# Optimization experiments

Measured on AMD Instinct MI355X. Metric: run time of the kernel, lower is better.

The kernel has to match this reference:

```python
import jax, jax.numpy as jnp
import numpy as np

N_NODES = 50000
N_EDGES = 800000
D = 64


def setup_inputs() -> dict:
    key = jax.random.key(0)
    ks = jax.random.split(key, 8)
    scale = 1.0 / np.sqrt(D)
    x = jax.random.normal(ks[0], (N_NODES, D), dtype=jnp.float32)
    edge_index = jax.random.randint(ks[1], (2, N_EDGES), 0, N_NODES, dtype=jnp.int64)
    W1_root = jax.random.normal(ks[2], (D, D), dtype=jnp.float32) * scale
    W1_nbr = jax.random.normal(ks[3], (D, D), dtype=jnp.float32) * scale
    b1 = jnp.zeros((D,), dtype=jnp.float32)
    W2_root = jax.random.normal(ks[4], (D, D), dtype=jnp.float32) * scale
    W2_nbr = jax.random.normal(ks[5], (D, D), dtype=jnp.float32) * scale
    b2 = jnp.zeros((D,), dtype=jnp.float32)
    return {"x": x, "edge_index": edge_index,
            "W1_root": W1_root, "W1_nbr": W1_nbr, "b1": b1,
            "W2_root": W2_root, "W2_nbr": W2_nbr, "b2": b2}


def graph_conv(x, src, dst, W_root, W_nbr, b, n_nodes):
    # sum-aggregate neighbor features: msg j->i uses x[src], scattered to dst
    agg = jax.ops.segment_sum(x[src], dst, num_segments=n_nodes)  # [N, D]
    return x @ W_root + agg @ W_nbr + b


def reference(x, edge_index, W1_root, W1_nbr, b1, W2_root, W2_nbr, b2):
    src, dst = edge_index[0], edge_index[1]
    n = x.shape[0]
    h = jax.nn.relu(graph_conv(x, src, dst, W1_root, W1_nbr, b1, n))
    out = graph_conv(h, src, dst, W2_root, W2_nbr, b2, n)
    return out
```

## Files before the change

kernel.cpp:

```cpp
#include <hip/hip_runtime.h>

#define N_NODES 50000
#define N_EDGES 800000
#define D 64
#define NBUCKETS 782
#define NPB 64
#define BCAP 2048
#define SBLOCKS 256
#define CHUNK (N_EDGES / SBLOCKS)
#define MB ((N_NODES + 63) / 64)

__device__ __forceinline__ unsigned short f2bf(float f) {
    unsigned u = __float_as_uint(f);
    return (unsigned short)((u + 0x7fffu + ((u >> 16) & 1u)) >> 16);
}
__device__ __forceinline__ float bflo(unsigned u) {
    return __uint_as_float(u << 16);
}
__device__ __forceinline__ float bfhi(unsigned u) {
    return __uint_as_float(u & 0xffff0000u);
}

__device__ __forceinline__ void scatter_body(
    const int* __restrict__ src, const int* __restrict__ dst,
    int* __restrict__ cursorPad, int* __restrict__ staged,
    char* smem, int bid, int t) {
    int* hist = (int*)smem;
    int* curs = (int*)(smem + 3200);
    int* pk   = (int*)(smem + 6400);
    unsigned short* bk = (unsigned short*)(smem + 6400 + 12500);
    for (int i = t; i < NBUCKETS; i += 256) hist[i] = 0;
    __syncthreads();
    int lo = bid * CHUNK;
    for (int i = t; i < CHUNK; i += 256) {
        int d = dst[lo + i];
        int s = src[lo + i];
        pk[i] = (s << 6) | (d & 63);
        bk[i] = (unsigned short)(d >> 6);
        atomicAdd(&hist[d >> 6], 1);
    }
    __syncthreads();
    for (int k = t; k < NBUCKETS; k += 256)
        if (hist[k] > 0)
            curs[k] = k * BCAP + atomicAdd(&cursorPad[k * 16], hist[k]);
    __syncthreads();
    for (int i = t; i < CHUNK; i += 256) {
        int b = bk[i];
        int pos = atomicAdd(&curs[b], 1);
        staged[pos] = pk[i];
    }
}

__global__ void __launch_bounds__(256) csr_build_kernel(
    const int* __restrict__ cursorPad, const int* __restrict__ staged,
    int* __restrict__ csr, int* __restrict__ startA, int* __restrict__ endA) {
    __shared__ int deg[NPB];
    __shared__ int sc[NPB];
    __shared__ int curs[NPB];
    __shared__ int lcsr[BCAP];
    int k = blockIdx.x;
    int t = threadIdx.x;
    int base = k * BCAP;
    int cnt  = cursorPad[k * 16];
    if (t < NPB) deg[t] = 0;
    __syncthreads();
    for (int i = t; i < cnt; i += 256)
        atomicAdd(&deg[staged[base + i] & 63], 1);
    __syncthreads();
    int v = (t < NPB) ? deg[t] : 0;
    if (t < NPB) sc[t] = v;
    __syncthreads();
#pragma unroll
    for (int d = 1; d < NPB; d <<= 1) {
        int u = (t < NPB && t >= d) ? sc[t - d] : 0;
        __syncthreads();
        if (t < NPB) sc[t] += u;
        __syncthreads();
    }
    if (t < NPB) {
        int start = sc[t] - v;
        int node = k * NPB + t;
        if (node < N_NODES) {
            startA[node] = base + start;
            endA[node]   = base + start + v;
        }
        curs[t] = start;
    }
    __syncthreads();
    for (int i = t; i < cnt; i += 256) {
        int e = staged[base + i];
        int pos = atomicAdd(&curs[e & 63], 1);
        lcsr[pos] = e >> 6;
    }
    __syncthreads();
    for (int i = t; i < cnt; i += 256)
        csr[base + i] = lcsr[i];
}

template<int XBF>
__device__ __forceinline__ void gemm_body(
    const float* __restrict__ Xf, const unsigned short* __restrict__ Xb,
    const float* __restrict__ Wr, const float* __restrict__ Wn,
    float* __restrict__ outR, unsigned short* __restrict__ outN,
    int node0, int tid, char* smem) {
    float (*sXT)[D] = (float(*)[D])smem;
    float (*sWr)[D] = (float(*)[D])(smem + 16384);
    float (*sWn)[D] = (float(*)[D])(smem + 32768);

#pragma unroll
    for (int i = 0; i < 4; i++) {
        int idx = tid + 256 * i;
        ((float4*)sWr)[idx] = ((const float4*)Wr)[idx];
        ((float4*)sWn)[idx] = ((const float4*)Wn)[idx];
    }
    int nd = tid & 63;
    int gn = min(node0 + nd, N_NODES - 1);
    if (XBF) {
#pragma unroll
        for (int pass = 0; pass < 2; pass++) {
            int kg = (tid >> 6) + pass * 4;
            int k0 = kg * 8;
            uint4 ux = *(const uint4*)(Xb + (size_t)gn * D + k0);
            sXT[k0 + 0][nd] = bflo(ux.x); sXT[k0 + 1][nd] = bfhi(ux.x);
            sXT[k0 + 2][nd] = bflo(ux.y); sXT[k0 + 3][nd] = bfhi(ux.y);
            sXT[k0 + 4][nd] = bflo(ux.z); sXT[k0 + 5][nd] = bfhi(ux.z);
            sXT[k0 + 6][nd] = bflo(ux.w); sXT[k0 + 7][nd] = bfhi(ux.w);
        }
    } else {
        const float4* X4 = (const float4*)Xf;
#pragma unroll
        for (int pass = 0; pass < 4; pass++) {
            int kq = (tid >> 6) + pass * 4;
            float4 v = X4[gn * 16 + kq];
            sXT[kq * 4 + 0][nd] = v.x; sXT[kq * 4 + 1][nd] = v.y;
            sXT[kq * 4 + 2][nd] = v.z; sXT[kq * 4 + 3][nd] = v.w;
        }
    }
    __syncthreads();

    int nq = tid >> 4;
    int cq = tid & 15;
    float accR[4][4];
    float accN[4][4];
#pragma unroll
    for (int i = 0; i < 4; i++)
#pragma unroll
        for (int jj = 0; jj < 4; jj++) { accR[i][jj] = 0.f; accN[i][jj] = 0.f; }

#pragma unroll 16
    for (int k = 0; k < D; k++) {
        float4 xv = *(const float4*)&sXT[k][nq * 4];
        float4 wr = *(const float4*)&sWr[k][cq * 4];
        float4 wn = *(const float4*)&sWn[k][cq * 4];
        float xs[4] = {xv.x, xv.y, xv.z, xv.w};
        float rs[4] = {wr.x, wr.y, wr.z, wr.w};
        float ns[4] = {wn.x, wn.y, wn.z, wn.w};
#pragma unroll
        for (int i = 0; i < 4; i++)
#pragma unroll
            for (int jj = 0; jj < 4; jj++) {
                accR[i][jj] = fmaf(xs[i], rs[jj], accR[i][jj]);
                accN[i][jj] = fmaf(xs[i], ns[jj], accN[i][jj]);
            }
    }

    float4* outR4 = (float4*)outR;
#pragma unroll
    for (int i = 0; i < 4; i++) {
        int node = node0 + nq * 4 + i;
        if (node < N_NODES) {
            float4 r;
            r.x = accR[i][0]; r.y = accR[i][1];
            r.z = accR[i][2]; r.w = accR[i][3];
            outR4[node * 16 + cq] = r;
            ushort4 rb;
            rb.x = f2bf(accN[i][0]); rb.y = f2bf(accN[i][1]);
            rb.z = f2bf(accN[i][2]); rb.w = f2bf(accN[i][3]);
            *(ushort4*)(outN + (size_t)node * D + cq * 4) = rb;
        }
    }
}

__global__ void __launch_bounds__(256) scatter_gemm1(
    const int* __restrict__ src, const int* __restrict__ dst,
    int* __restrict__ cursorPad, int* __restrict__ staged,
    const float* __restrict__ X,
    const float* __restrict__ Wr, const float* __restrict__ Wn,
    float* __restrict__ xr, unsigned short* __restrict__ xn) {
    __shared__ char smem[49152];
    if (blockIdx.x < SBLOCKS) {
        scatter_body(src, dst, cursorPad, staged, smem, blockIdx.x, threadIdx.x);
    } else {
        gemm_body<0>(X, (const unsigned short*)0, Wr, Wn, xr, xn,
                     (blockIdx.x - SBLOCKS) * 64, threadIdx.x, smem);
    }
}

__global__ void __launch_bounds__(256) gemm2(
    const unsigned short* __restrict__ Xb,
    const float* __restrict__ Wr, const float* __restrict__ Wn,
    float* __restrict__ hr, unsigned short* __restrict__ hn) {
    __shared__ char smem[49152];
    gemm_body<1>((const float*)0, Xb, Wr, Wn, hr, hn,
                 blockIdx.x * 64, threadIdx.x, smem);
}

template<int RELU, int OUTBF>
__global__ void __launch_bounds__(256) gather_fused(
    const unsigned short* __restrict__ Gsrc, const float* __restrict__ Root,
    const float* __restrict__ bias,
    const int* __restrict__ startA, const int* __restrict__ endA,
    const int* __restrict__ csr,
    float* __restrict__ outF, unsigned short* __restrict__ outB) {
    int tid = threadIdx.x;
    int wave = tid >> 6, lane = tid & 63;
    int node = blockIdx.x * 4 + wave;
    int sub = lane >> 3, fq = lane & 7;
    int j0 = startA[node], je = endA[node];
    float a0=0.f,a1=0.f,a2=0.f,a3=0.f,a4=0.f,a5=0.f,a6=0.f,a7=0.f;
    for (int jb = j0; jb < je; jb += 64) {
        int idx = jb + lane;
        int p = csr[idx < je ? idx : (je - 1)];
        int m = min(64, je - jb);
        int b = 0;
        for (; b + 16 <= m; b += 16) {
            int i0 = __shfl(p, b + sub, 64);
            int i1 = __shfl(p, b + 8 + sub, 64);
            uint4 u0 = *(const uint4*)(Gsrc + i0 * D + fq * 8);
            uint4 u1 = *(const uint4*)(Gsrc + i1 * D + fq * 8);
            a0 += bflo(u0.x) + bflo(u1.x);  a1 += bfhi(u0.x) + bfhi(u1.x);
            a2 += bflo(u0.y) + bflo(u1.y);  a3 += bfhi(u0.y) + bfhi(u1.y);
            a4 += bflo(u0.z) + bflo(u1.z);  a5 += bfhi(u0.z) + bfhi(u1.z);
            a6 += bflo(u0.w) + bflo(u1.w);  a7 += bfhi(u0.w) + bfhi(u1.w);
        }
        for (; b < m; b += 8) {
            int sidx = b + sub;
            int scl = sidx < m ? sidx : (m - 1);
            int i0 = __shfl(p, scl, 64);
            if (sidx < m) {
                uint4 u = *(const uint4*)(Gsrc + i0 * D + fq * 8);
                a0 += bflo(u.x); a1 += bfhi(u.x);
                a2 += bflo(u.y); a3 += bfhi(u.y);
                a4 += bflo(u.z); a5 += bfhi(u.z);
                a6 += bflo(u.w); a7 += bfhi(u.w);
            }
        }
    }
#pragma unroll
    for (int mk = 8; mk <= 32; mk <<= 1) {
        a0 += __shfl_xor(a0, mk, 64); a1 += __shfl_xor(a1, mk, 64);
        a2 += __shfl_xor(a2, mk, 64); a3 += __shfl_xor(a3, mk, 64);
        a4 += __shfl_xor(a4, mk, 64); a5 += __shfl_xor(a5, mk, 64);
        a6 += __shfl_xor(a6, mk, 64); a7 += __shfl_xor(a7, mk, 64);
    }
    if (sub == 0) {
        const float* rp = Root + (size_t)node * D + fq * 8;
        float4 x0 = *(const float4*)rp;
        float4 x1 = *(const float4*)(rp + 4);
        float4 b0 = ((const float4*)bias)[fq * 2];
        float4 b1 = ((const float4*)bias)[fq * 2 + 1];
        float r0 = a0 + x0.x + b0.x, r1 = a1 + x0.y + b0.y;
        float r2 = a2 + x0.z + b0.z, r3 = a3 + x0.w + b0.w;
        float r4 = a4 + x1.x + b1.x, r5 = a5 + x1.y + b1.y;
        float r6 = a6 + x1.z + b1.z, r7 = a7 + x1.w + b1.w;
        if (RELU) {
            r0 = fmaxf(r0, 0.f); r1 = fmaxf(r1, 0.f);
            r2 = fmaxf(r2, 0.f); r3 = fmaxf(r3, 0.f);
            r4 = fmaxf(r4, 0.f); r5 = fmaxf(r5, 0.f);
            r6 = fmaxf(r6, 0.f); r7 = fmaxf(r7, 0.f);
        }
        if (OUTBF) {
            uint4 u;
            u.x = (unsigned)f2bf(r0) | ((unsigned)f2bf(r1) << 16);
            u.y = (unsigned)f2bf(r2) | ((unsigned)f2bf(r3) << 16);
            u.z = (unsigned)f2bf(r4) | ((unsigned)f2bf(r5) << 16);
            u.w = (unsigned)f2bf(r6) | ((unsigned)f2bf(r7) << 16);
            *(uint4*)(outB + (size_t)node * D + fq * 8) = u;
        } else {
            float4 w0; w0.x = r0; w0.y = r1; w0.z = r2; w0.w = r3;
            float4 w1; w1.x = r4; w1.y = r5; w1.z = r6; w1.w = r7;
            *(float4*)(outF + (size_t)node * D + fq * 8) = w0;
            *(float4*)(outF + (size_t)node * D + fq * 8 + 4) = w1;
        }
    }
}

extern "C" void kernel_launch(void* const* d_in, const int* in_sizes, int n_in,
                              void* d_out, int out_size, void* d_ws, size_t ws_size,
                              hipStream_t stream) {
    const float* x   = (const float*)d_in[0];
    const int*   edg = (const int*)d_in[1];
    const float* W1r = (const float*)d_in[2];
    const float* W1n = (const float*)d_in[3];
    const float* b1  = (const float*)d_in[4];
    const float* W2r = (const float*)d_in[5];
    const float* W2n = (const float*)d_in[6];
    const float* b2  = (const float*)d_in[7];
    float* out = (float*)d_out;

    const int* src = edg;
    const int* dst = edg + N_EDGES;

    int* W              = (int*)d_ws;
    int* cursorPad      = W;
    int* staged         = W + NBUCKETS * 16;
    int* csr            = staged + NBUCKETS * BCAP;
    int* startA         = csr + NBUCKETS * BCAP;
    int* endA           = startA + N_NODES;
    float* xr           = (float*)(endA + N_NODES);
    unsigned short* xn  = (unsigned short*)(xr + (size_t)N_NODES * D);
    unsigned short* hbf = xn + (size_t)N_NODES * D;
    float* hr           = (float*)(hbf + (size_t)N_NODES * D);
    unsigned short* hn  = (unsigned short*)(hr + (size_t)N_NODES * D);

    hipMemsetAsync(cursorPad, 0, NBUCKETS * 16 * sizeof(int), stream);

    scatter_gemm1<<<SBLOCKS + MB, 256, 0, stream>>>(
        src, dst, cursorPad, staged, x, W1r, W1n, xr, xn);

    csr_build_kernel<<<NBUCKETS, 256, 0, stream>>>(cursorPad, staged, csr,
                                                   startA, endA);

    const int GB = N_NODES / 4;

    gather_fused<1, 1><<<GB, 256, 0, stream>>>(
        xn, xr, b1, startA, endA, csr, (float*)0, hbf);

    gemm2<<<MB, 256, 0, stream>>>(hbf, W2r, W2n, hr, hn);

    gather_fused<0, 0><<<GB, 256, 0, stream>>>(
        hn, hr, b2, startA, endA, csr, out, (unsigned short*)0);
}
```

Before: 175.4 us.

## Replace scalar FMA dense GEMMs with bf16 MFMA and pre-transposed bf16 weights

Swaps the LDS-staged scalar FMA GEMM for one built on the 16x16x32 bf16 MFMA instruction, with each wave computing 16 rows directly from registers. A new prep kernel converts and transposes all four weight matrices to bf16 and also clears the bucket counters, replacing the memset. This removes the shared-memory staging and the FP32 FMA work and cuts the LDS footprint of the fused scatter kernel. In exchange, the root branch now runs at bf16 input precision, and the output stores become scalar and strided per lane instead of vectorised.

```diff
diff --git a/kernel.cpp b/kernel.cpp
--- a/kernel.cpp
+++ b/kernel.cpp
@@ -10,6 +10,9 @@
 #define CHUNK (N_EDGES / SBLOCKS)
 #define MB ((N_NODES + 63) / 64)
 
+typedef short bf16x8 __attribute__((ext_vector_type(8)));
+typedef float f32x4  __attribute__((ext_vector_type(4)));
+
 __device__ __forceinline__ unsigned short f2bf(float f) {
     unsigned u = __float_as_uint(f);
     return (unsigned short)((u + 0x7fffu + ((u >> 16) & 1u)) >> 16);
@@ -19,6 +22,24 @@
 }
 __device__ __forceinline__ float bfhi(unsigned u) {
     return __uint_as_float(u & 0xffff0000u);
+}
+
+__global__ void __launch_bounds__(256) prep_kernel(
+    const float* __restrict__ W1r, const float* __restrict__ W1n,
+    const float* __restrict__ W2r, const float* __restrict__ W2n,
+    int* __restrict__ cursorPad, unsigned short* __restrict__ wt) {
+    int t = threadIdx.x;
+    if (blockIdx.x == 4) {
+        for (int i = t; i < NBUCKETS * 16; i += 256) cursorPad[i] = 0;
+        return;
+    }
+    const float* Wsrc = blockIdx.x == 0 ? W1r : blockIdx.x == 1 ? W1n
+                      : blockIdx.x == 2 ? W2r : W2n;
+    unsigned short* dstw = wt + blockIdx.x * D * D;
+    for (int i = t; i < D * D; i += 256) {
+        int k = i >> 6, c = i & 63;
+        dstw[c * D + k] = f2bf(Wsrc[i]);
+    }
 }
 
 __device__ __forceinline__ void scatter_body(
@@ -49,6 +70,87 @@
         int pos = atomicAdd(&curs[b], 1);
         staged[pos] = pk[i];
     }
+}
+
+template<int XBF>
+__device__ __forceinline__ void gemm_mfma_body(
+    const float* __restrict__ Xf, const unsigned short* __restrict__ Xb,
+    const unsigned short* __restrict__ Wtr, const unsigned short* __restrict__ Wtn,
+    float* __restrict__ outR, unsigned short* __restrict__ outN,
+    int node0, int tid) {
+    int wave = tid >> 6, lane = tid & 63;
+    int rbase = node0 + wave * 16;
+    int rrow  = lane & 15;
+    int kg    = lane >> 4;
+    int row   = min(rbase + rrow, N_NODES - 1);
+
+    bf16x8 a0, a1;
+    if (XBF) {
+        a0 = *(const bf16x8*)(Xb + (size_t)row * D + kg * 8);
+        a1 = *(const bf16x8*)(Xb + (size_t)row * D + 32 + kg * 8);
+    } else {
+        const float* xp = Xf + (size_t)row * D + kg * 8;
+#pragma unroll
+        for (int j = 0; j < 8; j++) a0[j] = (short)f2bf(xp[j]);
+#pragma unroll
+        for (int j = 0; j < 8; j++) a1[j] = (short)f2bf(xp[32 + j]);
+    }
+
+    f32x4 accR[4], accN[4];
+#pragma unroll
+    for (int t = 0; t < 4; t++) {
+        accR[t][0] = 0.f; accR[t][1] = 0.f; accR[t][2] = 0.f; accR[t][3] = 0.f;
+        accN[t][0] = 0.f; accN[t][1] = 0.f; accN[t][2] = 0.f; accN[t][3] = 0.f;
+    }
+
+#pragma unroll
+    for (int t = 0; t < 4; t++) {
+        int c = t * 16 + rrow;
+        bf16x8 br0 = *(const bf16x8*)(Wtr + c * D + kg * 8);
+        bf16x8 br1 = *(const bf16x8*)(Wtr + c * D + 32 + kg * 8);
+        bf16x8 bn0 = *(const bf16x8*)(Wtn + c * D + kg * 8);
+        bf16x8 bn1 = *(const bf16x8*)(Wtn + c * D + 32 + kg * 8);
+        accR[t] = __builtin_amdgcn_mfma_f32_16x16x32_bf16(a0, br0, accR[t], 0, 0, 0);
+        accR[t] = __builtin_amdgcn_mfma_f32_16x16x32_bf16(a1, br1, accR[t], 0, 0, 0);
+        accN[t] = __builtin_amdgcn_mfma_f32_16x16x32_bf16(a0, bn0, accN[t], 0, 0, 0);
+        accN[t] = __builtin_amdgcn_mfma_f32_16x16x32_bf16(a1, bn1, accN[t], 0, 0, 0);
+    }
+
+#pragma unroll
+    for (int t = 0; t < 4; t++) {
+#pragma unroll
+        for (int i = 0; i < 4; i++) {
+            int n = rbase + kg * 4 + i;
+            if (n < N_NODES) {
+                int c = t * 16 + rrow;
+                outR[(size_t)n * D + c] = accR[t][i];
+                outN[(size_t)n * D + c] = f2bf(accN[t][i]);
+            }
+        }
+    }
+}
+
+__global__ void __launch_bounds__(256) scatter_gemm1(
+    const int* __restrict__ src, const int* __restrict__ dst,
+    int* __restrict__ cursorPad, int* __restrict__ staged,
+    const float* __restrict__ X, const unsigned short* __restrict__ wt,
+    float* __restrict__ xr, unsigned short* __restrict__ xn) {
+    __shared__ char smem[25600];
+    if (blockIdx.x < SBLOCKS) {
+        scatter_body(src, dst, cursorPad, staged, smem, blockIdx.x, threadIdx.x);
+    } else {
+        gemm_mfma_body<0>(X, (const unsigned short*)0,
+                          wt + 0 * D * D, wt + 1 * D * D,
+                          xr, xn, (blockIdx.x - SBLOCKS) * 64, threadIdx.x);
+    }
+}
+
+__global__ void __launch_bounds__(256) gemm2(
+    const unsigned short* __restrict__ Xb, const unsigned short* __restrict__ wt,
+    float* __restrict__ hr, unsigned short* __restrict__ hn) {
+    gemm_mfma_body<1>((const float*)0, Xb,
+                      wt + 2 * D * D, wt + 3 * D * D,
+                      hr, hn, blockIdx.x * 64, threadIdx.x);
 }
 
 __global__ void __launch_bounds__(256) csr_build_kernel(
@@ -95,114 +197,6 @@
     __syncthreads();
     for (int i = t; i < cnt; i += 256)
         csr[base + i] = lcsr[i];
-}
-
-template<int XBF>
-__device__ __forceinline__ void gemm_body(
-    const float* __restrict__ Xf, const unsigned short* __restrict__ Xb,
-    const float* __restrict__ Wr, const float* __restrict__ Wn,
-    float* __restrict__ outR, unsigned short* __restrict__ outN,
-    int node0, int tid, char* smem) {
-    float (*sXT)[D] = (float(*)[D])smem;
-    float (*sWr)[D] = (float(*)[D])(smem + 16384);
-    float (*sWn)[D] = (float(*)[D])(smem + 32768);
-
-#pragma unroll
-    for (int i = 0; i < 4; i++) {
-        int idx = tid + 256 * i;
-        ((float4*)sWr)[idx] = ((const float4*)Wr)[idx];
-        ((float4*)sWn)[idx] = ((const float4*)Wn)[idx];
-    }
-    int nd = tid & 63;
-    int gn = min(node0 + nd, N_NODES - 1);
-    if (XBF) {
-#pragma unroll
-        for (int pass = 0; pass < 2; pass++) {
-            int kg = (tid >> 6) + pass * 4;
-            int k0 = kg * 8;
-            uint4 ux = *(const uint4*)(Xb + (size_t)gn * D + k0);
-            sXT[k0 + 0][nd] = bflo(ux.x); sXT[k0 + 1][nd] = bfhi(ux.x);
-            sXT[k0 + 2][nd] = bflo(ux.y); sXT[k0 + 3][nd] = bfhi(ux.y);
-            sXT[k0 + 4][nd] = bflo(ux.z); sXT[k0 + 5][nd] = bfhi(ux.z);
-            sXT[k0 + 6][nd] = bflo(ux.w); sXT[k0 + 7][nd] = bfhi(ux.w);
-        }
-    } else {
-        const float4* X4 = (const float4*)Xf;
-#pragma unroll
-        for (int pass = 0; pass < 4; pass++) {
-            int kq = (tid >> 6) + pass * 4;
-            float4 v = X4[gn * 16 + kq];
-            sXT[kq * 4 + 0][nd] = v.x; sXT[kq * 4 + 1][nd] = v.y;
-            sXT[kq * 4 + 2][nd] = v.z; sXT[kq * 4 + 3][nd] = v.w;
-        }
-    }
-    __syncthreads();
-
-    int nq = tid >> 4;
-    int cq = tid & 15;
-    float accR[4][4];
-    float accN[4][4];
-#pragma unroll
-    for (int i = 0; i < 4; i++)
-#pragma unroll
-        for (int jj = 0; jj < 4; jj++) { accR[i][jj] = 0.f; accN[i][jj] = 0.f; }
-
-#pragma unroll 16
-    for (int k = 0; k < D; k++) {
-        float4 xv = *(const float4*)&sXT[k][nq * 4];
-        float4 wr = *(const float4*)&sWr[k][cq * 4];
-        float4 wn = *(const float4*)&sWn[k][cq * 4];
-        float xs[4] = {xv.x, xv.y, xv.z, xv.w};
-        float rs[4] = {wr.x, wr.y, wr.z, wr.w};
-        float ns[4] = {wn.x, wn.y, wn.z, wn.w};
-#pragma unroll
-        for (int i = 0; i < 4; i++)
-#pragma unroll
-            for (int jj = 0; jj < 4; jj++) {
-                accR[i][jj] = fmaf(xs[i], rs[jj], accR[i][jj]);
-                accN[i][jj] = fmaf(xs[i], ns[jj], accN[i][jj]);
-            }
-    }
-
-    float4* outR4 = (float4*)outR;
-#pragma unroll
-    for (int i = 0; i < 4; i++) {
-        int node = node0 + nq * 4 + i;
-        if (node < N_NODES) {
-            float4 r;
-            r.x = accR[i][0]; r.y = accR[i][1];
-            r.z = accR[i][2]; r.w = accR[i][3];
-            outR4[node * 16 + cq] = r;
-            ushort4 rb;
-            rb.x = f2bf(accN[i][0]); rb.y = f2bf(accN[i][1]);
-            rb.z = f2bf(accN[i][2]); rb.w = f2bf(accN[i][3]);
-            *(ushort4*)(outN + (size_t)node * D + cq * 4) = rb;
-        }
-    }
-}
-
-__global__ void __launch_bounds__(256) scatter_gemm1(
-    const int* __restrict__ src, const int* __restrict__ dst,
-    int* __restrict__ cursorPad, int* __restrict__ staged,
-    const float* __restrict__ X,
-    const float* __restrict__ Wr, const float* __restrict__ Wn,
-    float* __restrict__ xr, unsigned short* __restrict__ xn) {
-    __shared__ char smem[49152];
-    if (blockIdx.x < SBLOCKS) {
-        scatter_body(src, dst, cursorPad, staged, smem, blockIdx.x, threadIdx.x);
-    } else {
-        gemm_body<0>(X, (const unsigned short*)0, Wr, Wn, xr, xn,
-                     (blockIdx.x - SBLOCKS) * 64, threadIdx.x, smem);
-    }
-}
-
-__global__ void __launch_bounds__(256) gemm2(
-    const unsigned short* __restrict__ Xb,
-    const float* __restrict__ Wr, const float* __restrict__ Wn,
-    float* __restrict__ hr, unsigned short* __restrict__ hn) {
-    __shared__ char smem[49152];
-    gemm_body<1>((const float*)0, Xb, Wr, Wn, hr, hn,
-                 blockIdx.x * 64, threadIdx.x, smem);
 }
 
 template<int RELU, int OUTBF>
@@ -312,11 +306,12 @@
     unsigned short* hbf = xn + (size_t)N_NODES * D;
     float* hr           = (float*)(hbf + (size_t)N_NODES * D);
     unsigned short* hn  = (unsigned short*)(hr + (size_t)N_NODES * D);
-
-    hipMemsetAsync(cursorPad, 0, NBUCKETS * 16 * sizeof(int), stream);
+    unsigned short* wt  = hn + (size_t)N_NODES * D;
+
+    prep_kernel<<<5, 256, 0, stream>>>(W1r, W1n, W2r, W2n, cursorPad, wt);
 
     scatter_gemm1<<<SBLOCKS + MB, 256, 0, stream>>>(
-        src, dst, cursorPad, staged, x, W1r, W1n, xr, xn);
+        src, dst, cursorPad, staged, x, wt, xr, xn);
 
     csr_build_kernel<<<NBUCKETS, 256, 0, stream>>>(cursorPad, staged, csr,
                                                    startA, endA);
@@ -326,7 +321,7 @@
     gather_fused<1, 1><<<GB, 256, 0, stream>>>(
         xn, xr, b1, startA, endA, csr, (float*)0, hbf);
 
-    gemm2<<<MB, 256, 0, stream>>>(hbf, W2r, W2n, hr, hn);
+    gemm2<<<MB, 256, 0, stream>>>(hbf, wt, hr, hn);
 
     gather_fused<0, 0><<<GB, 256, 0, stream>>>(
         hn, hr, b2, startA, endA, csr, out, (unsigned short*)0);
```

Measured after the change: 173.4 us. Within noise of the previous version (-1.1%).
